# Performance work log

Hardware: AMD Instinct MI355X
Metric: run time of the kernel (lower is better)

## Reference

```python
import jax, jax.numpy as jnp
import numpy as np
import math

N = 8192
IN_FEATURES = 512
OUT_FEATURES = 512
BUCKET = 4          # self.bucket -> number of hash buckets
NHASH = 1           # nHashTable hardcoded to 1 in forward
NEG = -9e15         # sentinel used by the original module


def setup_inputs() -> dict:
    key = jax.random.key(0)
    k_in, k_adj, k_rot, k_kw, k_vw = jax.random.split(key, 5)
    inp = jax.random.normal(k_in, (N, IN_FEATURES), dtype=jnp.float32)
    adj = jax.random.randint(k_adj, (N, N), 0, 2, dtype=jnp.int32)
    rotations_rands = jax.random.normal(k_rot, (NHASH, OUT_FEATURES, BUCKET // 2), dtype=jnp.float32)
    # xavier_uniform with gain=1.414 for (in, out) matrices
    limit = 1.414 * math.sqrt(6.0 / (IN_FEATURES + OUT_FEATURES))
    kW = jax.random.uniform(k_kw, (IN_FEATURES, OUT_FEATURES), minval=-limit, maxval=limit, dtype=jnp.float32)
    vW = jax.random.uniform(k_vw, (IN_FEATURES, OUT_FEATURES), minval=-limit, maxval=limit, dtype=jnp.float32)
    return {"input": inp, "adj": adj, "rotations_rands": rotations_rands, "kW": kW, "vW": vW}


def reference(input, adj, rotations_rands, kW, vW):
    kh = input @ kW                      # [N, H]
    vh = input @ vW                      # [N, H]
    H = kh.shape[1]

    # LSH bucketing: rotate keys, argmax over [r, -r] -> bucket id per node
    rv = jnp.einsum('nh,thb->tnb', kh, rotations_rands)   # [1, N, B/2]
    rv = jnp.concatenate([rv, -rv], axis=-1)              # [1, N, B]
    buckets = jnp.argmax(rv, axis=2)[0]                   # [N]

    # Original scatters per-bucket kh@kh.T blocks into a dense NxN matrix
    # initialized at NEG; equivalent to masking full scores by same-bucket.
    same_bucket = buckets[:, None] == buckets[None, :]    # [N, N]
    scores = (kh @ kh.T) / jnp.sqrt(jnp.asarray(H, kh.dtype))
    K = jnp.where(same_bucket, scores, NEG)

    attention = jnp.where(adj > 0, K, NEG)
    attention = jax.nn.softmax(attention, axis=1)
    # dropout is identity in eval mode (reference runs in eval)
    h_prime = attention @ vh                              # [N, H]
    return jax.nn.elu(h_prime)                            # concat=True -> ELU
```

## Files before the change

### kernel.cpp

```cpp
#include <hip/hip_runtime.h>
#include <hip/hip_bf16.h>
#include <math.h>

#define N_NODES 8192
#define FEAT 512
#define NEGV -9e15f
#define VHPT_W 8704

typedef __attribute__((ext_vector_type(8))) short short8;
typedef __attribute__((ext_vector_type(4))) float floatx4;

#define OFF_KH    0UL
#define OFF_VH    16777216UL
#define OFF_KHP   33554432UL
#define OFF_VHPT  42074112UL
#define OFF_MASK  50987008UL
#define OFF_S     59375616UL
#define OFF_PERM  109707264UL
#define OFF_FLAGS 109740032UL
#define OFF_BUCK  109772800UL
#define OFF_META  109805568UL
#define OFF_CMEAN 109806592UL
#define WS_NEEDED 109808640UL
#define CAP_S     25165824L

#define OFF_AHI   (OFF_S)
#define OFF_ALO   (OFF_S + 8388608UL)
#define OFF_WKHI  (OFF_S + 16777216UL)
#define OFF_WKLO  (OFF_S + 17301504UL)
#define OFF_WVHI  (OFF_S + 17825792UL)
#define OFF_WVLO  (OFF_S + 18350080UL)
#define OFF_CW    (OFF_MASK)

static __device__ __forceinline__ unsigned short f2bf_bits(float x) {
  __hip_bfloat16 h = __float2bfloat16(x);
  unsigned short u;
  __builtin_memcpy(&u, &h, 2);
  return u;
}
static __device__ __forceinline__ float bf_bits2f(unsigned short u) {
  __hip_bfloat16 h;
  __builtin_memcpy(&h, &u, 2);
  return __bfloat162float(h);
}

__global__ __launch_bounds__(256) void convert_input(
    const float* __restrict__ A, __hip_bfloat16* __restrict__ Ahi,
    __hip_bfloat16* __restrict__ Alo) {
  const long idx = ((long)blockIdx.x * 256 + threadIdx.x) * 4;
  const float4 v = *(const float4*)&A[idx];
  const float vv[4] = {v.x, v.y, v.z, v.w};
  ushort4 hi, lo;
  unsigned short* hp = (unsigned short*)&hi;
  unsigned short* lp = (unsigned short*)&lo;
#pragma unroll
  for (int e = 0; e < 4; e++) {
    unsigned short h = f2bf_bits(vv[e]);
    hp[e] = h;
    lp[e] = f2bf_bits(vv[e] - bf_bits2f(h));
  }
  *(ushort4*)&Ahi[idx] = hi;
  *(ushort4*)&Alo[idx] = lo;
}

__global__ __launch_bounds__(256) void convert_w(
    const float* __restrict__ kW, const float* __restrict__ vW,
    __hip_bfloat16* __restrict__ WkhiT, __hip_bfloat16* __restrict__ WkloT,
    __hip_bfloat16* __restrict__ WvhiT, __hip_bfloat16* __restrict__ WvloT) {
  __shared__ float tile[64][65];
  const int z = blockIdx.z;
  const float* __restrict__ W = z ? vW : kW;
  __hip_bfloat16* __restrict__ HiT = z ? WvhiT : WkhiT;
  __hip_bfloat16* __restrict__ LoT = z ? WvloT : WkloT;
  const int k0 = blockIdx.x * 64, n0 = blockIdx.y * 64;
  const int t = threadIdx.x;
#pragma unroll
  for (int s = 0; s < 16; s++) {
    int idx = t + s * 256;
    int r = idx >> 6, c = idx & 63;
    tile[r][c] = W[(long)(k0 + r) * FEAT + n0 + c];
  }
  __syncthreads();
#pragma unroll
  for (int s = 0; s < 16; s++) {
    int idx = t + s * 256;
    int a = idx >> 6, b = idx & 63;
    float w = tile[b][a];
    unsigned short h = f2bf_bits(w);
    unsigned short l = f2bf_bits(w - bf_bits2f(h));
    __builtin_memcpy(&HiT[(long)(n0 + a) * FEAT + k0 + b], &h, 2);
    __builtin_memcpy(&LoT[(long)(n0 + a) * FEAT + k0 + b], &l, 2);
  }
}

__global__ __launch_bounds__(256) void mfma_dual(
    const __hip_bfloat16* __restrict__ Ahi, const __hip_bfloat16* __restrict__ Alo,
    const __hip_bfloat16* __restrict__ WkhiT, const __hip_bfloat16* __restrict__ WkloT,
    const __hip_bfloat16* __restrict__ WvhiT, const __hip_bfloat16* __restrict__ WvloT,
    float* __restrict__ kh, float* __restrict__ vh) {
  const int z = blockIdx.z;
  const __hip_bfloat16* __restrict__ WhiT = z ? WvhiT : WkhiT;
  const __hip_bfloat16* __restrict__ WloT = z ? WvloT : WkloT;
  float* __restrict__ outp = z ? vh : kh;
  const int ti = blockIdx.x, tj = blockIdx.y;
  __shared__ __align__(16) __hip_bfloat16 Ah[128 * 32];
  __shared__ __align__(16) __hip_bfloat16 Al[128 * 32];
  __shared__ __align__(16) __hip_bfloat16 Wh[128 * 32];
  __shared__ __align__(16) __hip_bfloat16 Wl[128 * 32];
  const int t = threadIdx.x;
  const int lane = t & 63, w = t >> 6;
  const int wm = (w >> 1) * 64, wn = (w & 1) * 64;
  const int quad = lane >> 4, ln = lane & 15;
  const int qr = quad * 8;
  floatx4 acc[4][4];
#pragma unroll
  for (int mi = 0; mi < 4; mi++)
#pragma unroll
    for (int ni = 0; ni < 4; ni++) acc[mi][ni] = (floatx4)0.f;
  for (int k0 = 0; k0 < FEAT; k0 += 32) {
    __syncthreads();
#pragma unroll
    for (int s = 0; s < 2; s++) {
      int c = t + s * 256;
      int row = c >> 2, off8 = (c & 3) * 8;
      *(int4*)&Ah[row * 32 + off8] =
          *(const int4*)&Ahi[(long)(ti * 128 + row) * FEAT + k0 + off8];
      *(int4*)&Al[row * 32 + off8] =
          *(const int4*)&Alo[(long)(ti * 128 + row) * FEAT + k0 + off8];
      *(int4*)&Wh[row * 32 + off8] =
          *(const int4*)&WhiT[(long)(tj * 128 + row) * FEAT + k0 + off8];
      *(int4*)&Wl[row * 32 + off8] =
          *(const int4*)&WloT[(long)(tj * 128 + row) * FEAT + k0 + off8];
    }
    __syncthreads();
    short8 ah[4], al[4], bh[4], bl[4];
#pragma unroll
    for (int mi = 0; mi < 4; mi++) {
      ah[mi] = *(const short8*)&Ah[(wm + mi * 16 + ln) * 32 + qr];
      al[mi] = *(const short8*)&Al[(wm + mi * 16 + ln) * 32 + qr];
    }
#pragma unroll
    for (int ni = 0; ni < 4; ni++) {
      bh[ni] = *(const short8*)&Wh[(wn + ni * 16 + ln) * 32 + qr];
      bl[ni] = *(const short8*)&Wl[(wn + ni * 16 + ln) * 32 + qr];
    }
#pragma unroll
    for (int mi = 0; mi < 4; mi++)
#pragma unroll
      for (int ni = 0; ni < 4; ni++) {
        acc[mi][ni] = __builtin_amdgcn_mfma_f32_16x16x32_bf16(
            ah[mi], bh[ni], acc[mi][ni], 0, 0, 0);
        acc[mi][ni] = __builtin_amdgcn_mfma_f32_16x16x32_bf16(
            ah[mi], bl[ni], acc[mi][ni], 0, 0, 0);
        acc[mi][ni] = __builtin_amdgcn_mfma_f32_16x16x32_bf16(
            al[mi], bh[ni], acc[mi][ni], 0, 0, 0);
      }
  }
#pragma unroll
  for (int mi = 0; mi < 4; mi++)
#pragma unroll
    for (int ni = 0; ni < 4; ni++) {
      int cc = tj * 128 + wn + ni * 16 + ln;
#pragma unroll
      for (int reg = 0; reg < 4; reg++) {
        int r = ti * 128 + wm + mi * 16 + quad * 4 + reg;
        outp[(long)r * FEAT + cc] = acc[mi][ni][reg];
      }
    }
}

__global__ __launch_bounds__(64) void cw_kernel(
    const float* __restrict__ kW, const float* __restrict__ rot,
    double* __restrict__ cw) {
  const int f = blockIdx.x;
  const int lane = threadIdx.x;
  double r0 = 0.0, r1 = 0.0;
  for (int h = lane; h < FEAT; h += 64) {
    double a = (double)kW[(long)f * FEAT + h];
    r0 += a * (double)rot[2 * h];
    r1 += a * (double)rot[2 * h + 1];
  }
#pragma unroll
  for (int off = 32; off > 0; off >>= 1) {
    r0 += __shfl_down(r0, off);
    r1 += __shfl_down(r1, off);
  }
  if (lane == 0) {
    cw[2 * f] = r0;
    cw[2 * f + 1] = r1;
  }
}

__global__ __launch_bounds__(64) void rv_bucket_kernel(
    const float* __restrict__ input, const double* __restrict__ cw,
    int* __restrict__ buckets) {
  const int i = blockIdx.x;
  const int lane = threadIdx.x;
  double r0 = 0.0, r1 = 0.0;
  for (int f = lane; f < FEAT; f += 64) {
    double a = (double)input[(long)i * FEAT + f];
    r0 += a * cw[2 * f];
    r1 += a * cw[2 * f + 1];
  }
#pragma unroll
  for (int off = 32; off > 0; off >>= 1) {
    r0 += __shfl_down(r0, off);
    r1 += __shfl_down(r1, off);
  }
  if (lane == 0) {
    int b = 0;
    double best = r0;
    if (r1 > best)  { best = r1;  b = 1; }
    if (-r0 > best) { best = -r0; b = 2; }
    if (-r1 > best) { best = -r1; b = 3; }
    buckets[i] = b;
  }
}

__global__ __launch_bounds__(256) void sort_kernel(
    const int* __restrict__ buckets, int* __restrict__ perm,
    int* __restrict__ meta) {
  __shared__ int lc[256][4];
  __shared__ int start[256][4];
  const int t = threadIdx.x;
  const int base = t * 32;
  int c0 = 0, c1 = 0, c2 = 0, c3 = 0;
  for (int k = 0; k < 32; k++) {
    int b = buckets[base + k];
    c0 += (b == 0); c1 += (b == 1); c2 += (b == 2); c3 += (b == 3);
  }
  lc[t][0] = c0; lc[t][1] = c1; lc[t][2] = c2; lc[t][3] = c3;
  __syncthreads();
  if (t == 0) {
    int tot[4] = {0, 0, 0, 0};
    for (int b = 0; b < 4; b++)
      for (int i = 0; i < 256; i++) tot[b] += lc[i][b];
    int boff[5];
    boff[0] = 0;
    for (int b = 0; b < 4; b++) boff[b + 1] = boff[b] + tot[b];
    int run[4];
    for (int b = 0; b < 4; b++) run[b] = boff[b];
    for (int i = 0; i < 256; i++)
      for (int b = 0; b < 4; b++) { start[i][b] = run[b]; run[b] += lc[i][b]; }
    for (int b = 0; b < 5; b++) meta[b] = boff[b];
    long so = 0;
    int po = 0;
    for (int b = 0; b < 4; b++) {
      int pad = ((tot[b] + 127) >> 7) << 7;
      meta[5 + b] = pad;
      meta[9 + b] = (int)so;
      meta[14 + b] = po;
      so += (long)pad * pad;
      po += pad;
    }
    meta[13] = (int)so;
    meta[18] = po;
    if (so > CAP_S)
      for (int b = 0; b < 4; b++) meta[5 + b] = 0;
  }
  __syncthreads();
  int s0 = start[t][0], s1 = start[t][1], s2 = start[t][2], s3 = start[t][3];
  for (int k = 0; k < 32; k++) {
    int i = base + k;
    int b = buckets[i];
    int pos = (b == 0) ? s0++ : ((b == 1) ? s1++ : ((b == 2) ? s2++ : s3++));
    perm[pos] = i;
  }
}

__global__ __launch_bounds__(256) void gather_khp_kernel(
    const float* __restrict__ kh, const int* __restrict__ perm,
    __hip_bfloat16* __restrict__ khp) {
  const int g = blockIdx.x;
  const int t = threadIdx.x;
  if (g < N_NODES) {
    const int p = perm[g];
    const float2 v = *(const float2*)&kh[(long)p * FEAT + 2 * t];
    khp[(long)g * FEAT + 2 * t] = __float2bfloat16(v.x);
    khp[(long)g * FEAT + 2 * t + 1] = __float2bfloat16(v.y);
  } else {
    khp[(long)g * FEAT + 2 * t] = __float2bfloat16(0.f);
    khp[(long)g * FEAT + 2 * t + 1] = __float2bfloat16(0.f);
  }
}

__global__ __launch_bounds__(256) void transpose_vhpT_kernel(
    const float* __restrict__ vh, const int* __restrict__ perm,
    const int* __restrict__ meta, __hip_bfloat16* __restrict__ vhpT) {
  __shared__ float tile[64][65];
  const int g0 = blockIdx.x * 64;
  const int f0 = blockIdx.y * 64;
  const int t = threadIdx.x;
#pragma unroll
  for (int s = 0; s < 16; s++) {
    int idx = t + s * 256;
    int r = idx >> 6, c = idx & 63;
    int pos = g0 + r;
    int b = (pos >= meta[15]) + (pos >= meta[16]) + (pos >= meta[17]);
    int local = pos - meta[14 + b];
    int n_b = meta[b + 1] - meta[b];
    float v = 0.f;
    if (local < n_b) v = vh[(long)perm[meta[b] + local] * FEAT + f0 + c];
    tile[r][c] = v;
  }
  __syncthreads();
#pragma unroll
  for (int s = 0; s < 16; s++) {
    int idx = t + s * 256;
    int fr = idx >> 6, gc = idx & 63;
    vhpT[(long)(f0 + fr) * VHPT_W + g0 + gc] = __float2bfloat16(tile[gc][fr]);
  }
}

__global__ __launch_bounds__(256) void maskpack_kernel(
    const int* __restrict__ adj, const int* __restrict__ perm,
    const int* __restrict__ meta, unsigned long long* __restrict__ maskbits) {
  __shared__ int adj_lds[N_NODES];
  const int g = blockIdx.x;
  const int t = threadIdx.x;
  const int b = (g >= meta[1]) + (g >= meta[2]) + (g >= meta[3]);
  const int boff = meta[b];
  const int n_b = meta[b + 1] - boff;
  const int padded = meta[5 + b];
  const int i = perm[g];
  const int* arow = adj + (long)i * N_NODES;
#pragma unroll
  for (int s = 0; s < 8; s++) {
    int idx = (t + s * 256) * 4;
    *(int4*)&adj_lds[idx] = *(const int4*)&arow[idx];
  }
  __syncthreads();
  const int lane = t & 63, w = t >> 6;
  for (int jj0 = w * 64; jj0 < padded; jj0 += 256) {
    int jj = jj0 + lane;
    int pred = 0;
    if (jj < n_b) pred = adj_lds[perm[boff + jj]] > 0;
    unsigned long long mword = __ballot(pred);
    if (lane == 0) maskbits[(long)g * 128 + (jj0 >> 6)] = mword;
  }
}

__global__ __launch_bounds__(256) void colmean_kernel(
    const float* __restrict__ vh, float* __restrict__ cmean) {
  const int j0 = blockIdx.x * 128;
  const int f = threadIdx.x * 2;
  float a0 = 0.f, a1 = 0.f;
  for (int j = j0; j < j0 + 128; j++) {
    float2 v = *(const float2*)&vh[(long)j * FEAT + f];
    a0 += v.x; a1 += v.y;
  }
  atomicAdd(&cmean[f], a0);
  atomicAdd(&cmean[f + 1], a1);
}

__global__ __launch_bounds__(256) void s_gemm(
    const __hip_bfloat16* __restrict__ khp, const int* __restrict__ meta,
    const unsigned long long* __restrict__ maskbits,
    __hip_bfloat16* __restrict__ S) {
  const int b = blockIdx.z;
  const int padded = meta[5 + b];
  const int ti = blockIdx.x, tj = blockIdx.y;
  if (ti * 128 >= padded || tj * 128 >= padded) return;
  const int boff = meta[b];
  const long soff = meta[9 + b];
  __shared__ __align__(16) __hip_bfloat16 As[128 * 32];
  __shared__ __align__(16) __hip_bfloat16 Bs[128 * 32];
  const int t = threadIdx.x;
  const int lane = t & 63, w = t >> 6;
  const int wm = (w >> 1) * 64, wn = (w & 1) * 64;
  const int quad = lane >> 4, ln = lane & 15;
  const int qr = quad * 8;
  floatx4 acc[4][4];
#pragma unroll
  for (int mi = 0; mi < 4; mi++)
#pragma unroll
    for (int ni = 0; ni < 4; ni++) acc[mi][ni] = (floatx4)0.f;
  const long a_g0 = boff + ti * 128;
  const long b_g0 = boff + tj * 128;
  for (int k0 = 0; k0 < FEAT; k0 += 32) {
    __syncthreads();
#pragma unroll
    for (int s = 0; s < 2; s++) {
      int c = t + s * 256;
      int row = c >> 2, off8 = (c & 3) * 8;
      *(int4*)&As[row * 32 + off8] =
          *(const int4*)&khp[(a_g0 + row) * FEAT + k0 + off8];
      *(int4*)&Bs[row * 32 + off8] =
          *(const int4*)&khp[(b_g0 + row) * FEAT + k0 + off8];
    }
    __syncthreads();
    short8 af[4], bfr[4];
#pragma unroll
    for (int mi = 0; mi < 4; mi++)
      af[mi] = *(const short8*)&As[(wm + mi * 16 + ln) * 32 + qr];
#pragma unroll
    for (int ni = 0; ni < 4; ni++)
      bfr[ni] = *(const short8*)&Bs[(wn + ni * 16 + ln) * 32 + qr];
#pragma unroll
    for (int mi = 0; mi < 4; mi++)
#pragma unroll
      for (int ni = 0; ni < 4; ni++)
        acc[mi][ni] = __builtin_amdgcn_mfma_f32_16x16x32_bf16(
            af[mi], bfr[ni], acc[mi][ni], 0, 0, 0);
  }
  const float scale = 0.04419417382415922f;
#pragma unroll
  for (int mi = 0; mi < 4; mi++) {
#pragma unroll
    for (int ni = 0; ni < 4; ni++) {
      int cb = tj * 128 + wn + ni * 16;
#pragma unroll
      for (int reg = 0; reg < 4; reg++) {
        int r = ti * 128 + wm + mi * 16 + quad * 4 + reg;
        unsigned long long wbits = maskbits[(long)(boff + r) * 128 + (cb >> 6)];
        int bit = (int)((wbits >> ((cb & 63) + ln)) & 1ULL);
        float v = acc[mi][ni][reg] * scale;
        S[soff + (long)r * padded + cb + ln] =
            __float2bfloat16(bit ? v : NEGV);
      }
    }
  }
}

__global__ __launch_bounds__(256) void softmax_kernel(
    __hip_bfloat16* __restrict__ S, const int* __restrict__ meta,
    int* __restrict__ flags) {
  const int g = blockIdx.x;
  const int b = (g >= meta[1]) + (g >= meta[2]) + (g >= meta[3]);
  const int boff = meta[b];
  const int padded = meta[5 + b];
  const long soff = meta[9 + b];
  __hip_bfloat16* row = S + soff + (long)(g - boff) * padded;
  __shared__ float red[256];
  __shared__ float pb[8192];
  const int t = threadIdx.x;
  float m = -INFINITY;
  for (int j0 = t * 8; j0 < padded; j0 += 2048) {
    union { short8 v; unsigned short u[8]; } pk;
    pk.v = *(const short8*)&row[j0];
#pragma unroll
    for (int e = 0; e < 8; e++) {
      float s = bf_bits2f(pk.u[e]);
      pb[j0 + e] = s;
      m = fmaxf(m, s);
    }
  }
  red[t] = m;
  __syncthreads();
#pragma unroll
  for (int o = 128; o > 0; o >>= 1) {
    if (t < o) red[t] = fmaxf(red[t], red[t + o]);
    __syncthreads();
  }
  m = red[0];
  __syncthreads();
  if (m < -8e15f) {
    if (t == 0) flags[g] = 1;
    union { short8 v; unsigned short u[8]; } zz;
#pragma unroll
    for (int e = 0; e < 8; e++) zz.u[e] = 0;
    for (int j0 = t * 8; j0 < padded; j0 += 2048) *(short8*)&row[j0] = zz.v;
    return;
  }
  if (t == 0) flags[g] = 0;
  float sum = 0.f;
  for (int j0 = t * 8; j0 < padded; j0 += 2048) {
#pragma unroll
    for (int e = 0; e < 8; e++) {
      float ex = expf(pb[j0 + e] - m);
      pb[j0 + e] = ex;
      sum += ex;
    }
  }
  red[t] = sum;
  __syncthreads();
#pragma unroll
  for (int o = 128; o > 0; o >>= 1) {
    if (t < o) red[t] += red[t + o];
    __syncthreads();
  }
  const float inv = 1.f / red[0];
  for (int j0 = t * 8; j0 < padded; j0 += 2048) {
    union { short8 v; unsigned short u[8]; } pk;
#pragma unroll
    for (int e = 0; e < 8; e++) pk.u[e] = f2bf_bits(pb[j0 + e] * inv);
    *(short8*)&row[j0] = pk.v;
  }
}

__global__ __launch_bounds__(256) void pv_gemm(
    const __hip_bfloat16* __restrict__ S, const __hip_bfloat16* __restrict__ vhpT,
    const int* __restrict__ meta, float* __restrict__ O0,
    float* __restrict__ O1) {
  const int b = blockIdx.z >> 1;
  const int half = blockIdx.z & 1;
  const int padded = meta[5 + b];
  const int ti = blockIdx.x;
  if (ti * 128 >= padded) return;
  const int boff = meta[b];
  const int n_b = meta[b + 1] - boff;
  const long soff = meta[9 + b];
  const int poff = meta[14 + b];
  const int f0 = blockIdx.y * 128;
  const int khalf = padded >> 1;
  const int kstart = half * khalf;
  float* __restrict__ O = half ? O1 : O0;
  __shared__ __align__(16) __hip_bfloat16 As[128 * 32];
  __shared__ __align__(16) __hip_bfloat16 Bs[128 * 32];
  const int t = threadIdx.x;
  const int lane = t & 63, w = t >> 6;
  const int wm = (w >> 1) * 64, wn = (w & 1) * 64;
  const int quad = lane >> 4, ln = lane & 15;
  const int qr = quad * 8;
  floatx4 acc[4][4];
#pragma unroll
  for (int mi = 0; mi < 4; mi++)
#pragma unroll
    for (int ni = 0; ni < 4; ni++) acc[mi][ni] = (floatx4)0.f;
  const long r0 = (long)ti * 128;
  for (int k0 = kstart; k0 < kstart + khalf; k0 += 32) {
    __syncthreads();
#pragma unroll
    for (int s = 0; s < 2; s++) {
      int c = t + s * 256;
      int row = c >> 2, off8 = (c & 3) * 8;
      *(int4*)&As[row * 32 + off8] =
          *(const int4*)&S[soff + (r0 + row) * padded + k0 + off8];
      *(int4*)&Bs[row * 32 + off8] =
          *(const int4*)&vhpT[(long)(f0 + row) * VHPT_W + poff + k0 + off8];
    }
    __syncthreads();
    short8 af[4], bfr[4];
#pragma unroll
    for (int mi = 0; mi < 4; mi++)
      af[mi] = *(const short8*)&As[(wm + mi * 16 + ln) * 32 + qr];
#pragma unroll
    for (int ni = 0; ni < 4; ni++)
      bfr[ni] = *(const short8*)&Bs[(wn + ni * 16 + ln) * 32 + qr];
#pragma unroll
    for (int mi = 0; mi < 4; mi++)
#pragma unroll
      for (int ni = 0; ni < 4; ni++)
        acc[mi][ni] = __builtin_amdgcn_mfma_f32_16x16x32_bf16(
            af[mi], bfr[ni], acc[mi][ni], 0, 0, 0);
  }
#pragma unroll
  for (int mi = 0; mi < 4; mi++) {
#pragma unroll
    for (int reg = 0; reg < 4; reg++) {
      int r = ti * 128 + wm + mi * 16 + quad * 4 + reg;
      if (r < n_b) {
        long g = boff + r;
#pragma unroll
        for (int ni = 0; ni < 4; ni++) {
          int fc = f0 + wn + ni * 16 + ln;
          O[g * FEAT + fc] = acc[mi][ni][reg];
        }
      }
    }
  }
}

__global__ __launch_bounds__(256) void elu_scatter_kernel(
    const float* __restrict__ O0, const float* __restrict__ O1,
    const int* __restrict__ flags, const int* __restrict__ perm,
    const float* __restrict__ cmean, float* __restrict__ out) {
  const int g = blockIdx.x;
  const int f = threadIdx.x * 2;
  const int node = perm[g];
  float a0, a1;
  if (flags[g]) {
    a0 = cmean[f] * (1.f / (float)N_NODES);
    a1 = cmean[f + 1] * (1.f / (float)N_NODES);
  } else {
    float2 v0 = *(const float2*)&O0[(long)g * FEAT + f];
    float2 v1 = *(const float2*)&O1[(long)g * FEAT + f];
    a0 = v0.x + v1.x;
    a1 = v0.y + v1.y;
  }
  a0 = a0 > 0.f ? a0 : expm1f(a0);
  a1 = a1 > 0.f ? a1 : expm1f(a1);
  *(float2*)&out[(long)node * FEAT + f] = make_float2(a0, a1);
}

__global__ __launch_bounds__(256) void gemm_dual(
    const float* __restrict__ A, const float* __restrict__ Wk,
    const float* __restrict__ Wv, float* __restrict__ kh,
    float* __restrict__ vh) {
  __shared__ float As[32][33];
  __shared__ float Bk[32][33];
  __shared__ float Bv[32][33];
  const int tid = threadIdx.x;
  const int row0 = blockIdx.x * 32;
  const int col0 = blockIdx.y * 32;
  const int tx = tid & 15, ty = tid >> 4;
  float ck00 = 0.f, ck01 = 0.f, ck10 = 0.f, ck11 = 0.f;
  float cv00 = 0.f, cv01 = 0.f, cv10 = 0.f, cv11 = 0.f;
  for (int kt = 0; kt < FEAT; kt += 32) {
#pragma unroll
    for (int t = 0; t < 4; t++) {
      int e = tid + t * 256;
      int r = e >> 5, c = e & 31;
      As[r][c] = A[(long)(row0 + r) * FEAT + kt + c];
      Bk[r][c] = Wk[(long)(kt + r) * FEAT + col0 + c];
      Bv[r][c] = Wv[(long)(kt + r) * FEAT + col0 + c];
    }
    __syncthreads();
#pragma unroll
    for (int kk = 0; kk < 32; kk++) {
      float a0 = As[ty * 2][kk], a1 = As[ty * 2 + 1][kk];
      float bk0 = Bk[kk][tx * 2], bk1 = Bk[kk][tx * 2 + 1];
      float bv0 = Bv[kk][tx * 2], bv1 = Bv[kk][tx * 2 + 1];
      ck00 += a0 * bk0; ck01 += a0 * bk1;
      ck10 += a1 * bk0; ck11 += a1 * bk1;
      cv00 += a0 * bv0; cv01 += a0 * bv1;
      cv10 += a1 * bv0; cv11 += a1 * bv1;
    }
    __syncthreads();
  }
  const int r0 = row0 + ty * 2, c0 = col0 + tx * 2;
  kh[(long)r0 * FEAT + c0] = ck00;       kh[(long)r0 * FEAT + c0 + 1] = ck01;
  kh[(long)(r0 + 1) * FEAT + c0] = ck10; kh[(long)(r0 + 1) * FEAT + c0 + 1] = ck11;
  vh[(long)r0 * FEAT + c0] = cv00;       vh[(long)r0 * FEAT + c0 + 1] = cv01;
  vh[(long)(r0 + 1) * FEAT + c0] = cv10; vh[(long)(r0 + 1) * FEAT + c0 + 1] = cv11;
}

__global__ __launch_bounds__(64) void bucket_kernel(
    const float* __restrict__ kh, const float* __restrict__ rot,
    int* __restrict__ buckets) {
  const int i = blockIdx.x;
  const int lane = threadIdx.x;
  double r0 = 0.0, r1 = 0.0;
  for (int h = lane; h < FEAT; h += 64) {
    double a = (double)kh[(long)i * FEAT + h];
    r0 += a * (double)rot[2 * h];
    r1 += a * (double)rot[2 * h + 1];
  }
#pragma unroll
  for (int off = 32; off > 0; off >>= 1) {
    r0 += __shfl_down(r0, off);
    r1 += __shfl_down(r1, off);
  }
  if (lane == 0) {
    int b = 0;
    double best = r0;
    if (r1 > best)  { best = r1;  b = 1; }
    if (-r0 > best) { best = -r0; b = 2; }
    if (-r1 > best) { best = -r1; b = 3; }
    buckets[i] = b;
  }
}

__global__ __launch_bounds__(256) void attn_kernel(
    const float* __restrict__ kh, const float* __restrict__ vh,
    const int* __restrict__ adj, const int* __restrict__ buckets,
    float* __restrict__ out) {
  __shared__ float khi[FEAT];
  __shared__ float pbuf[N_NODES];
  __shared__ unsigned short jlist[N_NODES];
  __shared__ int cnt_sh;
  __shared__ float red[256];
  const int i = blockIdx.x;
  const int tid = threadIdx.x;
  if (tid == 0) cnt_sh = 0;
  for (int k = tid; k < FEAT; k += 256) khi[k] = kh[(long)i * FEAT + k];
  const int mybucket = buckets[i];
  __syncthreads();
  const int* adjrow = adj + (long)i * N_NODES;
  for (int j = tid; j < N_NODES; j += 256) {
    if (adjrow[j] > 0 && buckets[j] == mybucket) {
      int idx = atomicAdd(&cnt_sh, 1);
      jlist[idx] = (unsigned short)j;
    }
  }
  __syncthreads();
  const int cnt = cnt_sh;
  float mloc = -INFINITY;
  for (int idx = tid; idx < cnt; idx += 256) {
    int j = jlist[idx];
    const float4* kj = (const float4*)(kh + (long)j * FEAT);
    const float4* ki = (const float4*)khi;
    float acc = 0.f;
#pragma unroll 8
    for (int k = 0; k < FEAT / 4; k++) {
      float4 a = ki[k];
      float4 b = kj[k];
      acc += a.x * b.x + a.y * b.y + a.z * b.z + a.w * b.w;
    }
    float s = acc * 0.04419417382415922f;
    pbuf[idx] = s;
    mloc = fmaxf(mloc, s);
  }
  red[tid] = mloc;
  __syncthreads();
#pragma unroll
  for (int off = 128; off > 0; off >>= 1) {
    if (tid < off) red[tid] = fmaxf(red[tid], red[tid + off]);
    __syncthreads();
  }
  const float m = red[0];
  __syncthreads();
  float lloc = 0.f;
  for (int idx = tid; idx < cnt; idx += 256) {
    float p = expf(pbuf[idx] - m);
    pbuf[idx] = p;
    lloc += p;
  }
  red[tid] = lloc;
  __syncthreads();
#pragma unroll
  for (int off = 128; off > 0; off >>= 1) {
    if (tid < off) red[tid] += red[tid + off];
    __syncthreads();
  }
  const float l = red[0];
  __syncthreads();
  const int f = 2 * tid;
  float acc0 = 0.f, acc1 = 0.f;
  if (cnt > 0) {
#pragma unroll 4
    for (int idx = 0; idx < cnt; idx++) {
      int j = jlist[idx];
      float p = pbuf[idx];
      float2 v = *(const float2*)(vh + (long)j * FEAT + f);
      acc0 += p * v.x;
      acc1 += p * v.y;
    }
    float invl = 1.f / l;
    acc0 *= invl;
    acc1 *= invl;
  } else {
    for (int j = 0; j < N_NODES; j++) {
      float2 v = *(const float2*)(vh + (long)j * FEAT + f);
      acc0 += v.x;
      acc1 += v.y;
    }
    acc0 *= (1.f / (float)N_NODES);
    acc1 *= (1.f / (float)N_NODES);
  }
  acc0 = acc0 > 0.f ? acc0 : expm1f(acc0);
  acc1 = acc1 > 0.f ? acc1 : expm1f(acc1);
  *(float2*)(out + (long)i * FEAT + f) = make_float2(acc0, acc1);
}

extern "C" void kernel_launch(void* const* d_in, const int* in_sizes, int n_in,
                              void* d_out, int out_size, void* d_ws,
                              size_t ws_size, hipStream_t stream) {
  const float* input = (const float*)d_in[0];
  const int* adj = (const int*)d_in[1];
  const float* rot = (const float*)d_in[2];
  const float* kW = (const float*)d_in[3];
  const float* vW = (const float*)d_in[4];
  float* out = (float*)d_out;

  char* ws = (char*)d_ws;
  float* kh = (float*)(ws + OFF_KH);
  float* vh = (float*)(ws + OFF_VH);

  if (ws_size >= WS_NEEDED) {
    __hip_bfloat16* khp = (__hip_bfloat16*)(ws + OFF_KHP);
    __hip_bfloat16* vhpT = (__hip_bfloat16*)(ws + OFF_VHPT);
    unsigned long long* maskbits = (unsigned long long*)(ws + OFF_MASK);
    __hip_bfloat16* S = (__hip_bfloat16*)(ws + OFF_S);
    int* perm = (int*)(ws + OFF_PERM);
    int* flags = (int*)(ws + OFF_FLAGS);
    int* buckets = (int*)(ws + OFF_BUCK);
    int* meta = (int*)(ws + OFF_META);
    float* cmean = (float*)(ws + OFF_CMEAN);
    __hip_bfloat16* Ahi = (__hip_bfloat16*)(ws + OFF_AHI);
    __hip_bfloat16* Alo = (__hip_bfloat16*)(ws + OFF_ALO);
    __hip_bfloat16* WkhiT = (__hip_bfloat16*)(ws + OFF_WKHI);
    __hip_bfloat16* WkloT = (__hip_bfloat16*)(ws + OFF_WKLO);
    __hip_bfloat16* WvhiT = (__hip_bfloat16*)(ws + OFF_WVHI);
    __hip_bfloat16* WvloT = (__hip_bfloat16*)(ws + OFF_WVLO);
    double* cw = (double*)(ws + OFF_CW);
    float* O0 = (float*)(ws + OFF_KH);
    float* O1 = (float*)(ws + OFF_VH);

    convert_input<<<4096, 256, 0, stream>>>(input, Ahi, Alo);
    convert_w<<<dim3(8, 8, 2), 256, 0, stream>>>(kW, vW, WkhiT, WkloT, WvhiT,
                                                 WvloT);
    mfma_dual<<<dim3(64, 4, 2), 256, 0, stream>>>(Ahi, Alo, WkhiT, WkloT,
                                                  WvhiT, WvloT, kh, vh);
    cw_kernel<<<512, 64, 0, stream>>>(kW, rot, cw);
    rv_bucket_kernel<<<N_NODES, 64, 0, stream>>>(input, cw, buckets);
    sort_kernel<<<1, 256, 0, stream>>>(buckets, perm, meta);
    gather_khp_kernel<<<N_NODES + 128, 256, 0, stream>>>(kh, perm, khp);
    transpose_vhpT_kernel<<<dim3(VHPT_W / 64, FEAT / 64), 256, 0, stream>>>(
        vh, perm, meta, vhpT);
    maskpack_kernel<<<N_NODES, 256, 0, stream>>>(adj, perm, meta, maskbits);
    hipMemsetAsync(cmean, 0, FEAT * sizeof(float), stream);
    colmean_kernel<<<64, 256, 0, stream>>>(vh, cmean);
    s_gemm<<<dim3(64, 64, 4), 256, 0, stream>>>(khp, meta, maskbits, S);
    softmax_kernel<<<N_NODES, 256, 0, stream>>>(S, meta, flags);
    pv_gemm<<<dim3(64, 4, 8), 256, 0, stream>>>(S, vhpT, meta, O0, O1);
    elu_scatter_kernel<<<N_NODES, 256, 0, stream>>>(O0, O1, flags, perm, cmean,
                                                    out);
  } else {
    dim3 gemm_grid(N_NODES / 32, FEAT / 32);
    gemm_dual<<<gemm_grid, 256, 0, stream>>>(input, kW, vW, kh, vh);
    int* buckets = (int*)(vh + (long)N_NODES * FEAT);
    bucket_kernel<<<N_NODES, 64, 0, stream>>>(kh, rot, buckets);
    attn_kernel<<<N_NODES, 256, 0, stream>>>(kh, vh, adj, buckets, out);
  }
}
```

Baseline: 665.3 us.

## Fuse ELU scatter into PV GEMM, fold column mean into transpose, parallel-scan sort

The PV GEMM no longer splits K into two halves written to O0/O1 buffers. Each block now covers 128 rows by 64 features over the full K range and applies the ELU/flag fallback directly, scattering to the output. This removes the separate elu_scatter kernel and its intermediate round trip. The column mean is now computed from the transpose kernel's LDS tile with atomics, which removes colmean_kernel. The sort kernel replaces its serial single-thread prefix computation with a parallel Hillis-Steele scan. In exchange, the GEMM has smaller tiles and loses the K-split parallelism, and its output writes are scattered and uncoalesced.

```diff
diff --git a/kernel.cpp b/kernel.cpp
--- a/kernel.cpp
+++ b/kernel.cpp
@@ -220,8 +220,9 @@
 __global__ __launch_bounds__(256) void sort_kernel(
     const int* __restrict__ buckets, int* __restrict__ perm,
     int* __restrict__ meta) {
-  __shared__ int lc[256][4];
-  __shared__ int start[256][4];
+  __shared__ int lc[4][256];
+  __shared__ int sc[4][256];
+  __shared__ int boff_sh[5];
   const int t = threadIdx.x;
   const int base = t * 32;
   int c0 = 0, c1 = 0, c2 = 0, c3 = 0;
@@ -229,24 +230,28 @@
     int b = buckets[base + k];
     c0 += (b == 0); c1 += (b == 1); c2 += (b == 2); c3 += (b == 3);
   }
-  lc[t][0] = c0; lc[t][1] = c1; lc[t][2] = c2; lc[t][3] = c3;
-  __syncthreads();
+  lc[0][t] = c0; lc[1][t] = c1; lc[2][t] = c2; lc[3][t] = c3;
+  sc[0][t] = c0; sc[1][t] = c1; sc[2][t] = c2; sc[3][t] = c3;
+  __syncthreads();
+  for (int off = 1; off < 256; off <<= 1) {
+    int a0 = (t >= off) ? sc[0][t - off] : 0;
+    int a1 = (t >= off) ? sc[1][t - off] : 0;
+    int a2 = (t >= off) ? sc[2][t - off] : 0;
+    int a3 = (t >= off) ? sc[3][t - off] : 0;
+    __syncthreads();
+    sc[0][t] += a0; sc[1][t] += a1; sc[2][t] += a2; sc[3][t] += a3;
+    __syncthreads();
+  }
   if (t == 0) {
-    int tot[4] = {0, 0, 0, 0};
-    for (int b = 0; b < 4; b++)
-      for (int i = 0; i < 256; i++) tot[b] += lc[i][b];
     int boff[5];
     boff[0] = 0;
-    for (int b = 0; b < 4; b++) boff[b + 1] = boff[b] + tot[b];
-    int run[4];
-    for (int b = 0; b < 4; b++) run[b] = boff[b];
-    for (int i = 0; i < 256; i++)
-      for (int b = 0; b < 4; b++) { start[i][b] = run[b]; run[b] += lc[i][b]; }
-    for (int b = 0; b < 5; b++) meta[b] = boff[b];
+    for (int b = 0; b < 4; b++) boff[b + 1] = boff[b] + sc[b][255];
+    for (int b = 0; b < 5; b++) { meta[b] = boff[b]; boff_sh[b] = boff[b]; }
     long so = 0;
     int po = 0;
     for (int b = 0; b < 4; b++) {
-      int pad = ((tot[b] + 127) >> 7) << 7;
+      int tot = boff[b + 1] - boff[b];
+      int pad = ((tot + 127) >> 7) << 7;
       meta[5 + b] = pad;
       meta[9 + b] = (int)so;
       meta[14 + b] = po;
@@ -259,7 +264,10 @@
       for (int b = 0; b < 4; b++) meta[5 + b] = 0;
   }
   __syncthreads();
-  int s0 = start[t][0], s1 = start[t][1], s2 = start[t][2], s3 = start[t][3];
+  int s0 = boff_sh[0] + sc[0][t] - lc[0][t];
+  int s1 = boff_sh[1] + sc[1][t] - lc[1][t];
+  int s2 = boff_sh[2] + sc[2][t] - lc[2][t];
+  int s3 = boff_sh[3] + sc[3][t] - lc[3][t];
   for (int k = 0; k < 32; k++) {
     int i = base + k;
     int b = buckets[i];
@@ -286,8 +294,10 @@
 
 __global__ __launch_bounds__(256) void transpose_vhpT_kernel(
     const float* __restrict__ vh, const int* __restrict__ perm,
-    const int* __restrict__ meta, __hip_bfloat16* __restrict__ vhpT) {
+    const int* __restrict__ meta, __hip_bfloat16* __restrict__ vhpT,
+    float* __restrict__ cmean) {
   __shared__ float tile[64][65];
+  __shared__ float cred[4][64];
   const int g0 = blockIdx.x * 64;
   const int f0 = blockIdx.y * 64;
   const int t = threadIdx.x;
@@ -304,6 +314,17 @@
     tile[r][c] = v;
   }
   __syncthreads();
+  {
+    const int c = t & 63, seg = t >> 6;
+    float ps = 0.f;
+#pragma unroll
+    for (int rr = 0; rr < 16; rr++) ps += tile[seg * 16 + rr][c];
+    cred[seg][c] = ps;
+  }
+  __syncthreads();
+  if (t < 64)
+    atomicAdd(&cmean[f0 + t],
+              cred[0][t] + cred[1][t] + cred[2][t] + cred[3][t]);
 #pragma unroll
   for (int s = 0; s < 16; s++) {
     int idx = t + s * 256;
@@ -338,19 +359,6 @@
     unsigned long long mword = __ballot(pred);
     if (lane == 0) maskbits[(long)g * 128 + (jj0 >> 6)] = mword;
   }
-}
-
-__global__ __launch_bounds__(256) void colmean_kernel(
-    const float* __restrict__ vh, float* __restrict__ cmean) {
-  const int j0 = blockIdx.x * 128;
-  const int f = threadIdx.x * 2;
-  float a0 = 0.f, a1 = 0.f;
-  for (int j = j0; j < j0 + 128; j++) {
-    float2 v = *(const float2*)&vh[(long)j * FEAT + f];
-    a0 += v.x; a1 += v.y;
-  }
-  atomicAdd(&cmean[f], a0);
-  atomicAdd(&cmean[f + 1], a1);
 }
 
 __global__ __launch_bounds__(256) void s_gemm(
@@ -490,10 +498,10 @@
 
 __global__ __launch_bounds__(256) void pv_gemm(
     const __hip_bfloat16* __restrict__ S, const __hip_bfloat16* __restrict__ vhpT,
-    const int* __restrict__ meta, float* __restrict__ O0,
-    float* __restrict__ O1) {
-  const int b = blockIdx.z >> 1;
-  const int half = blockIdx.z & 1;
+    const int* __restrict__ meta, const int* __restrict__ perm,
+    const int* __restrict__ flags, const float* __restrict__ cmean,
+    float* __restrict__ out) {
+  const int b = blockIdx.z;
   const int padded = meta[5 + b];
   const int ti = blockIdx.x;
   if (ti * 128 >= padded) return;
@@ -501,24 +509,21 @@
   const int n_b = meta[b + 1] - boff;
   const long soff = meta[9 + b];
   const int poff = meta[14 + b];
-  const int f0 = blockIdx.y * 128;
-  const int khalf = padded >> 1;
-  const int kstart = half * khalf;
-  float* __restrict__ O = half ? O1 : O0;
+  const int f0 = blockIdx.y * 64;
   __shared__ __align__(16) __hip_bfloat16 As[128 * 32];
-  __shared__ __align__(16) __hip_bfloat16 Bs[128 * 32];
+  __shared__ __align__(16) __hip_bfloat16 Bs[64 * 32];
   const int t = threadIdx.x;
   const int lane = t & 63, w = t >> 6;
-  const int wm = (w >> 1) * 64, wn = (w & 1) * 64;
+  const int wm = w * 32;
   const int quad = lane >> 4, ln = lane & 15;
   const int qr = quad * 8;
-  floatx4 acc[4][4];
-#pragma unroll
-  for (int mi = 0; mi < 4; mi++)
+  floatx4 acc[2][4];
+#pragma unroll
+  for (int mi = 0; mi < 2; mi++)
 #pragma unroll
     for (int ni = 0; ni < 4; ni++) acc[mi][ni] = (floatx4)0.f;
   const long r0 = (long)ti * 128;
-  for (int k0 = kstart; k0 < kstart + khalf; k0 += 32) {
+  for (int k0 = 0; k0 < padded; k0 += 32) {
     __syncthreads();
 #pragma unroll
     for (int s = 0; s < 2; s++) {
@@ -526,61 +531,47 @@
       int row = c >> 2, off8 = (c & 3) * 8;
       *(int4*)&As[row * 32 + off8] =
           *(const int4*)&S[soff + (r0 + row) * padded + k0 + off8];
+    }
+    {
+      int row = t >> 2, off8 = (t & 3) * 8;
       *(int4*)&Bs[row * 32 + off8] =
           *(const int4*)&vhpT[(long)(f0 + row) * VHPT_W + poff + k0 + off8];
     }
     __syncthreads();
-    short8 af[4], bfr[4];
-#pragma unroll
-    for (int mi = 0; mi < 4; mi++)
+    short8 af[2], bfr[4];
+#pragma unroll
+    for (int mi = 0; mi < 2; mi++)
       af[mi] = *(const short8*)&As[(wm + mi * 16 + ln) * 32 + qr];
 #pragma unroll
     for (int ni = 0; ni < 4; ni++)
-      bfr[ni] = *(const short8*)&Bs[(wn + ni * 16 + ln) * 32 + qr];
-#pragma unroll
-    for (int mi = 0; mi < 4; mi++)
+      bfr[ni] = *(const short8*)&Bs[(ni * 16 + ln) * 32 + qr];
+#pragma unroll
+    for (int mi = 0; mi < 2; mi++)
 #pragma unroll
       for (int ni = 0; ni < 4; ni++)
         acc[mi][ni] = __builtin_amdgcn_mfma_f32_16x16x32_bf16(
             af[mi], bfr[ni], acc[mi][ni], 0, 0, 0);
   }
 #pragma unroll
-  for (int mi = 0; mi < 4; mi++) {
+  for (int mi = 0; mi < 2; mi++) {
 #pragma unroll
     for (int reg = 0; reg < 4; reg++) {
       int r = ti * 128 + wm + mi * 16 + quad * 4 + reg;
       if (r < n_b) {
-        long g = boff + r;
+        int g = boff + r;
+        int node = perm[g];
+        int fl = flags[g];
 #pragma unroll
         for (int ni = 0; ni < 4; ni++) {
-          int fc = f0 + wn + ni * 16 + ln;
-          O[g * FEAT + fc] = acc[mi][ni][reg];
+          int fc = f0 + ni * 16 + ln;
+          float v = fl ? cmean[fc] * (1.f / (float)N_NODES)
+                       : acc[mi][ni][reg];
+          v = v > 0.f ? v : expm1f(v);
+          out[(long)node * FEAT + fc] = v;
         }
       }
     }
   }
-}
-
-__global__ __launch_bounds__(256) void elu_scatter_kernel(
-    const float* __restrict__ O0, const float* __restrict__ O1,
-    const int* __restrict__ flags, const int* __restrict__ perm,
-    const float* __restrict__ cmean, float* __restrict__ out) {
-  const int g = blockIdx.x;
-  const int f = threadIdx.x * 2;
-  const int node = perm[g];
-  float a0, a1;
-  if (flags[g]) {
-    a0 = cmean[f] * (1.f / (float)N_NODES);
-    a1 = cmean[f + 1] * (1.f / (float)N_NODES);
-  } else {
-    float2 v0 = *(const float2*)&O0[(long)g * FEAT + f];
-    float2 v1 = *(const float2*)&O1[(long)g * FEAT + f];
-    a0 = v0.x + v1.x;
-    a1 = v0.y + v1.y;
-  }
-  a0 = a0 > 0.f ? a0 : expm1f(a0);
-  a1 = a1 > 0.f ? a1 : expm1f(a1);
-  *(float2*)&out[(long)node * FEAT + f] = make_float2(a0, a1);
 }
 
 __global__ __launch_bounds__(256) void gemm_dual(
@@ -774,8 +765,6 @@
     __hip_bfloat16* WvhiT = (__hip_bfloat16*)(ws + OFF_WVHI);
     __hip_bfloat16* WvloT = (__hip_bfloat16*)(ws + OFF_WVLO);
     double* cw = (double*)(ws + OFF_CW);
-    float* O0 = (float*)(ws + OFF_KH);
-    float* O1 = (float*)(ws + OFF_VH);
 
     convert_input<<<4096, 256, 0, stream>>>(input, Ahi, Alo);
     convert_w<<<dim3(8, 8, 2), 256, 0, stream>>>(kW, vW, WkhiT, WkloT, WvhiT,
@@ -786,16 +775,14 @@
     rv_bucket_kernel<<<N_NODES, 64, 0, stream>>>(input, cw, buckets);
     sort_kernel<<<1, 256, 0, stream>>>(buckets, perm, meta);
     gather_khp_kernel<<<N_NODES + 128, 256, 0, stream>>>(kh, perm, khp);
+    hipMemsetAsync(cmean, 0, FEAT * sizeof(float), stream);
     transpose_vhpT_kernel<<<dim3(VHPT_W / 64, FEAT / 64), 256, 0, stream>>>(
-        vh, perm, meta, vhpT);
+        vh, perm, meta, vhpT, cmean);
     maskpack_kernel<<<N_NODES, 256, 0, stream>>>(adj, perm, meta, maskbits);
-    hipMemsetAsync(cmean, 0, FEAT * sizeof(float), stream);
-    colmean_kernel<<<64, 256, 0, stream>>>(vh, cmean);
     s_gemm<<<dim3(64, 64, 4), 256, 0, stream>>>(khp, meta, maskbits, S);
     softmax_kernel<<<N_NODES, 256, 0, stream>>>(S, meta, flags);
-    pv_gemm<<<dim3(64, 4, 8), 256, 0, stream>>>(S, vhpT, meta, O0, O1);
-    elu_scatter_kernel<<<N_NODES, 256, 0, stream>>>(O0, O1, flags, perm, cmean,
-                                                    out);
+    pv_gemm<<<dim3(64, 8, 4), 256, 0, stream>>>(S, vhpT, meta, perm, flags,
+                                                cmean, out);
   } else {
     dim3 gemm_grid(N_NODES / 32, FEAT / 32);
     gemm_dual<<<gemm_grid, 256, 0, stream>>>(input, kW, vW, kh, vh);
```

Result: no change. 662.5 us (-0.4%).
